# Performance work log

Hardware: AMD Instinct MI355X
Metric: run time of the kernel (lower is better)

## Reference

```python
import jax, jax.numpy as jnp
import numpy as np

B, S, D, H, M = 2, 2048, 1024, 16, 4096  # batch, seqlen, dim, n_heads, max_seq_len
HD = D // H  # head_dim = 64
EPS = 1e-5


def layernorm(x, g, b):
    mu = jnp.mean(x, axis=-1, keepdims=True)
    var = jnp.mean((x - mu) ** 2, axis=-1, keepdims=True)
    return (x - mu) * jax.lax.rsqrt(var + EPS) * g + b


def setup_inputs() -> dict:
    key = jax.random.key(0)
    ks = jax.random.split(key, 5)
    x = jax.random.normal(ks[0], (B, S, D), jnp.float32)
    # causal mask: >=0 -> keep, negative -> drop (forward does att *= mask >= 0)
    i = jnp.arange(S)
    mask = jnp.where(i[None, :] <= i[:, None], 0, -1).astype(jnp.int32)[None, None]
    w1 = jax.random.normal(ks[1], (4 * D, D), jnp.float32) * (D ** -0.5)
    b1 = jnp.zeros((4 * D,), jnp.float32)
    w2 = jax.random.normal(ks[2], (D, D), jnp.float32) * (D ** -0.5)
    b2 = jnp.zeros((D,), jnp.float32)
    g1 = jnp.ones((D,), jnp.float32)
    beta1 = jnp.zeros((D,), jnp.float32)
    g2 = jnp.ones((D,), jnp.float32)
    beta2 = jnp.zeros((D,), jnp.float32)
    pos_w = jax.random.normal(ks[3], (2 * M - 1,), jnp.float32) * 0.02
    return dict(x=x, mask=mask, w1=w1, b1=b1, w2=w2, b2=b2,
                g1=g1, beta1=beta1, g2=g2, beta2=beta2, pos_w=pos_w)


def reference(x, mask, w1, b1, w2, b2, g1, beta1, g2, beta2, pos_w):
    # f1 + silu, split into gate u and q/k/v
    h = jax.nn.silu(x @ w1.T + b1)                      # [B,S,4D]
    u, q, k, v = jnp.split(h, 4, axis=-1)
    to_heads = lambda t: t.reshape(B, S, H, HD).transpose(0, 2, 1, 3)  # [B,H,S,HD]
    u, q, k, v = map(to_heads, (u, q, k, v))
    # relative positional bias: bias[i,j] = pos_w[M-1 + (j - i)]
    rel = jnp.arange(S)[None, :] - jnp.arange(S)[:, None]
    bias = pos_w[M - 1 + rel]                           # [S,S]
    att = jax.nn.silu(jnp.einsum('bhqd,bhkd->bhqk', q, k) + bias)
    att = att * (mask >= 0)                             # [B,H,S,S]
    y = jnp.einsum('bhqk,bhkd->bhqd', att, v) * u
    y = y.transpose(0, 2, 1, 3).reshape(B, S, D)
    y = layernorm(y, g1, beta1)
    y = y @ w2.T + b2
    return layernorm(y + x, g2, beta2)
```

## Files before the change

### kernel.cpp

```cpp
#include <hip/hip_runtime.h>
#include <hip/hip_bf16.h>

#define BN   2
#define SEQ  2048
#define DIM  1024
#define NH   16
#define HD   64
#define D4   4096
#define MAXS 4096

using bf16 = __hip_bfloat16;
typedef __bf16 bf16x8 __attribute__((ext_vector_type(8)));
typedef float  f32x4  __attribute__((ext_vector_type(4)));

__device__ __forceinline__ float bf2f(bf16 v){ return __bfloat162float(v); }
__device__ __forceinline__ bf16  f2bf(float v){ return __float2bfloat16(v); }
__device__ __forceinline__ float silu_f(float v){
  const float e = __expf(-v);
  return v * __builtin_amdgcn_rcpf(1.f + e);
}

__device__ __forceinline__ void async16(void* lds, const void* g){
  __builtin_amdgcn_global_load_lds((const __attribute__((address_space(1))) void*)g,
                                   (__attribute__((address_space(3))) void*)lds, 16, 0, 0);
}
__device__ __forceinline__ f32x4 mfma16(bf16x8 a, bf16x8 b, f32x4 c){
  return __builtin_amdgcn_mfma_f32_16x16x32_bf16(a, b, c, 0, 0, 0);
}

__global__ __launch_bounds__(256) void f2bk3(
    const float* __restrict__ a, bf16* __restrict__ ao, int na,
    const float* __restrict__ b, bf16* __restrict__ bo, int nb,
    const float* __restrict__ c, bf16* __restrict__ co)
{
  int i = (blockIdx.x * 256 + threadIdx.x) * 4;
  const float* in; bf16* out;
  if (i < na){ in = a; out = ao; }
  else if (i < na + nb){ in = b; out = bo; i -= na; }
  else { in = c; out = co; i -= na + nb; }
  const float4 v = *(const float4*)(in + i);
  bf16 t0 = f2bf(v.x), t1 = f2bf(v.y), t2 = f2bf(v.z), t3 = f2bf(v.w);
  ushort4 o;
  o.x = *(unsigned short*)&t0; o.y = *(unsigned short*)&t1;
  o.z = *(unsigned short*)&t2; o.w = *(unsigned short*)&t3;
  *(ushort4*)((unsigned short*)out + i) = o;
}

template<int NTOT>
__global__ __launch_bounds__(256) void gemm_bt(
    const bf16* __restrict__ A, const bf16* __restrict__ W,
    const float* __restrict__ bias, bf16* __restrict__ outb)
{
  constexpr int K = DIM;
  const int ntiles = NTOT / 128;
  const int m0 = (int)(blockIdx.x / ntiles) * 128;
  const int n0 = (int)(blockIdx.x % ntiles) * 128;
  __shared__ bf16 Al[128*32];
  __shared__ bf16 Bl[128*32];
  const int tid = threadIdx.x, wave = tid>>6, lane = tid&63;
  const int quad = lane>>4, l16 = lane&15;
  const int srow = lane>>2;
  const int sg   = ((lane&3) ^ ((lane>>3)&3)) * 8;
  const int wm = (wave>>1)*64, wn = (wave&1)*64;
  const int rkey = ((l16>>1)&3);

  f32x4 acc[4][4];
  #pragma unroll
  for (int i=0;i<4;i++)
    #pragma unroll
    for (int j=0;j<4;j++) acc[i][j] = (f32x4){0.f,0.f,0.f,0.f};

  const bf16* aB = A + m0*K;
  const bf16* wB = W + n0*K;

  for (int k0 = 0; k0 < K; k0 += 32){
    async16(&Al[wave*1024      ], aB + (wave*32      + srow)*K + k0 + sg);
    async16(&Al[wave*1024 + 512], aB + (wave*32 + 16 + srow)*K + k0 + sg);
    async16(&Bl[wave*1024      ], wB + (wave*32      + srow)*K + k0 + sg);
    async16(&Bl[wave*1024 + 512], wB + (wave*32 + 16 + srow)*K + k0 + sg);
    __syncthreads();
    bf16x8 af[4], bv[4];
    #pragma unroll
    for (int mt=0;mt<4;mt++) af[mt] = *(const bf16x8*)&Al[(wm+mt*16+l16)*32 + (quad ^ rkey)*8];
    #pragma unroll
    for (int nt=0;nt<4;nt++) bv[nt] = *(const bf16x8*)&Bl[(wn+nt*16+l16)*32 + (quad ^ rkey)*8];
    #pragma unroll
    for (int mt=0;mt<4;mt++)
      #pragma unroll
      for (int nt=0;nt<4;nt++)
        acc[mt][nt] = mfma16(af[mt], bv[nt], acc[mt][nt]);
    __syncthreads();
  }

  #pragma unroll
  for (int mt=0;mt<4;mt++){
    #pragma unroll
    for (int nt=0;nt<4;nt++){
      const int row = m0 + wm + mt*16 + quad*4;
      const int col = n0 + wn + nt*16 + l16;
      const float bvv = bias[col];
      #pragma unroll
      for (int r=0;r<4;r++){
        float v = silu_f(acc[mt][nt][r] + bvv);
        outb[(row+r)*NTOT + col] = f2bf(v);
      }
    }
  }
}

__global__ __launch_bounds__(256) void gemm_bt2(
    const bf16* __restrict__ A, const bf16* __restrict__ W,
    const float* __restrict__ bias, const float* __restrict__ resid,
    float* __restrict__ outf)
{
  constexpr int K = DIM, NTOT = DIM;
  const int ntiles = NTOT / 64;
  const int m0 = (int)(blockIdx.x / ntiles) * 128;
  const int n0 = (int)(blockIdx.x % ntiles) * 64;
  __shared__ bf16 Al[128*32];
  __shared__ bf16 Bl[64*32];
  const int tid = threadIdx.x, wave = tid>>6, lane = tid&63;
  const int quad = lane>>4, l16 = lane&15;
  const int srow = lane>>2;
  const int sg   = ((lane&3) ^ ((lane>>3)&3)) * 8;
  const int wm = wave*32;
  const int rkey = ((l16>>1)&3);

  f32x4 acc[2][4];
  #pragma unroll
  for (int i=0;i<2;i++)
    #pragma unroll
    for (int j=0;j<4;j++) acc[i][j] = (f32x4){0.f,0.f,0.f,0.f};

  const bf16* aB = A + m0*K;
  const bf16* wB = W + n0*K;

  for (int k0 = 0; k0 < K; k0 += 32){
    async16(&Al[wave*1024      ], aB + (wave*32      + srow)*K + k0 + sg);
    async16(&Al[wave*1024 + 512], aB + (wave*32 + 16 + srow)*K + k0 + sg);
    async16(&Bl[wave*512       ], wB + (wave*16      + srow)*K + k0 + sg);
    __syncthreads();
    bf16x8 af[2], bv[4];
    #pragma unroll
    for (int mt=0;mt<2;mt++) af[mt] = *(const bf16x8*)&Al[(wm+mt*16+l16)*32 + (quad ^ rkey)*8];
    #pragma unroll
    for (int nt=0;nt<4;nt++) bv[nt] = *(const bf16x8*)&Bl[(nt*16+l16)*32 + (quad ^ rkey)*8];
    #pragma unroll
    for (int mt=0;mt<2;mt++)
      #pragma unroll
      for (int nt=0;nt<4;nt++)
        acc[mt][nt] = mfma16(af[mt], bv[nt], acc[mt][nt]);
    __syncthreads();
  }

  #pragma unroll
  for (int mt=0;mt<2;mt++){
    #pragma unroll
    for (int nt=0;nt<4;nt++){
      const int row = m0 + wm + mt*16 + quad*4;
      const int col = n0 + nt*16 + l16;
      const float bvv = bias[col];
      #pragma unroll
      for (int r=0;r<4;r++){
        outf[(row+r)*NTOT + col] = acc[mt][nt][r] + bvv + resid[(row+r)*NTOT + col];
      }
    }
  }
}

__global__ __launch_bounds__(256) void vtrans(const bf16* __restrict__ h, bf16* __restrict__ vt)
{
  __shared__ bf16 t[64][65];
  const int bid = blockIdx.x;
  const int ct = bid & 15;
  const int st = (bid >> 4) & 31;
  const int b  = bid >> 9;
  const int s0 = st*64, c0 = ct*64;
  const int tid = threadIdx.x;
  #pragma unroll
  for (int i=0;i<16;i++){
    int idx = tid + i*256;
    int r = idx >> 6, c = idx & 63;
    t[r][c] = h[(b*SEQ + s0 + r)*D4 + 3*DIM + c0 + c];
  }
  __syncthreads();
  #pragma unroll
  for (int i=0;i<16;i++){
    int idx = tid + i*256;
    int c = idx >> 6, r = idx & 63;
    vt[((b*NH + ct)*HD + c)*SEQ + s0 + r] = t[r][c];
  }
}

__global__ __launch_bounds__(256) void attn(
    const bf16* __restrict__ h, const bf16* __restrict__ vt,
    const float* __restrict__ pw, bf16* __restrict__ y)
{
  const int bid = blockIdx.x;
  const int g  = (bid & 7) + ((bid >> 7) << 3);
  const int qp = (bid >> 3) & 15;
  const int hh = g & 15, b = g >> 4;
  __shared__ bf16 Kl[128*64];
  __shared__ bf16 Vl[64*128];
  __shared__ bf16 Pl[4][16*136];
  __shared__ float pwl[256];
  const int tid = threadIdx.x, wave = tid>>6, lane = tid&63;
  const int quad = lane>>4, l16 = lane&15;

  const bf16* kgb = h + b*SEQ*D4 + 2*DIM + hh*HD;
  const bf16* vgb = vt + (b*NH + hh)*HD*SEQ;
  const int krow8 = lane>>3;
  const int kgo   = ((lane&7) ^ krow8) * 8;
  const int vrow4 = lane>>4;

  #pragma unroll
  for (int pass = 0; pass < 2; ++pass){
    const int qt = pass ? (31 - qp) : qp;
    const int q0 = qt * 64;

    const bf16* qbase = h + (b*SEQ + q0 + wave*16 + l16)*D4 + DIM + hh*HD;
    bf16x8 qf[2];
    qf[0] = *(const bf16x8*)(qbase + quad*8);
    qf[1] = *(const bf16x8*)(qbase + 32 + quad*8);

    f32x4 oacc[4];
    #pragma unroll
    for (int nt=0;nt<4;nt++) oacc[nt] = (f32x4){0.f,0.f,0.f,0.f};

    const int kmax = q0 + 64;
    for (int k0 = 0; k0 < kmax; k0 += 128){
      #pragma unroll
      for (int t=0;t<4;t++)
        async16(&Kl[(wave*32 + t*8)*64], kgb + (k0 + wave*32 + t*8 + krow8)*D4 + kgo);
      #pragma unroll
      for (int t=0;t<4;t++){
        const int vg = ((lane&15) ^ (t*4 + vrow4)) * 8;
        async16(&Vl[(wave*16 + t*4)*128], vgb + (wave*16 + t*4 + vrow4)*SEQ + k0 + vg);
      }
      const int W0 = MAXS - 1 + k0 - q0 - 63;
      if (wave == 0) async16(&pwl[0], pw + W0 + lane*4);
      __syncthreads();

      f32x4 sacc[8];
      #pragma unroll
      for (int nt=0;nt<8;nt++) sacc[nt] = (f32x4){0.f,0.f,0.f,0.f};
      #pragma unroll
      for (int ks=0;ks<2;ks++){
        #pragma unroll
        for (int nt=0;nt<8;nt++){
          bf16x8 kf = *(const bf16x8*)&Kl[(nt*16 + l16)*64 + ((ks*4 + quad) ^ (l16&7))*8];
          sacc[nt] = mfma16(qf[ks], kf, sacc[nt]);
        }
      }
      const int li = wave*16 + quad*4;
      const int dq = q0 - k0;
      #pragma unroll
      for (int nt=0;nt<8;nt++){
        const int lj = nt*16 + l16;
        #pragma unroll
        for (int r=0;r<4;r++){
          const float bias = pwl[lj - (li+r) + 63];
          const float sv = silu_f(sacc[nt][r] + bias);
          const float v = (lj - (li+r) <= dq) ? sv : 0.f;
          Pl[wave][(quad*4+r)*136 + lj] = f2bf(v);
        }
      }

      #pragma unroll
      for (int ks=0;ks<4;ks++){
        bf16x8 pf = *(const bf16x8*)&Pl[wave][l16*136 + ks*32 + quad*8];
        #pragma unroll
        for (int nt=0;nt<4;nt++){
          bf16x8 vf = *(const bf16x8*)&Vl[(nt*16 + l16)*128 + ((ks*4 + quad) ^ l16)*8];
          oacc[nt] = mfma16(pf, vf, oacc[nt]);
        }
      }
      __syncthreads();
    }

    const int qrow = q0 + wave*16 + quad*4;
    #pragma unroll
    for (int nt=0;nt<4;nt++){
      const int c = hh*HD + nt*16 + l16;
      #pragma unroll
      for (int r=0;r<4;r++){
        const int srow = b*SEQ + qrow + r;
        const float uu = bf2f(h[srow*D4 + c]);
        y[srow*DIM + c] = f2bf(oacc[nt][r] * uu);
      }
    }
    __syncthreads();
  }
}

template<bool FP32IN, bool FP32OUT>
__global__ __launch_bounds__(256) void lnorm(const void* __restrict__ in,
    const float* __restrict__ g, const float* __restrict__ be, void* __restrict__ out)
{
  const int row = blockIdx.x;
  const int tid = threadIdx.x, wave = tid>>6, lane = tid&63;
  const int c0 = tid*4;
  float v[4];
  if (FP32IN){
    const float* p = (const float*)in + row*DIM + c0;
    #pragma unroll
    for (int j=0;j<4;j++) v[j] = p[j];
  } else {
    const bf16* p = (const bf16*)in + row*DIM + c0;
    #pragma unroll
    for (int j=0;j<4;j++) v[j] = bf2f(p[j]);
  }
  float s = 0.f, ss = 0.f;
  #pragma unroll
  for (int j=0;j<4;j++){ s += v[j]; ss += v[j]*v[j]; }
  #pragma unroll
  for (int off=32; off>0; off>>=1){
    s  += __shfl_down(s, off);
    ss += __shfl_down(ss, off);
  }
  __shared__ float red[8];
  if (lane==0){ red[wave] = s; red[4+wave] = ss; }
  __syncthreads();
  s  = red[0]+red[1]+red[2]+red[3];
  ss = red[4]+red[5]+red[6]+red[7];
  const float mu   = s * (1.f/DIM);
  const float var  = ss * (1.f/DIM) - mu*mu;
  const float rstd = rsqrtf(var + 1e-5f);
  #pragma unroll
  for (int j=0;j<4;j++){
    const int c = c0 + j;
    const float o = (v[j]-mu)*rstd*g[c] + be[c];
    if (FP32OUT) ((float*)out)[row*DIM + c] = o;
    else         ((bf16*)out)[row*DIM + c] = f2bf(o);
  }
}

extern "C" void kernel_launch(void* const* d_in, const int* in_sizes, int n_in,
                              void* d_out, int out_size, void* d_ws, size_t ws_size,
                              hipStream_t stream)
{
  const float* x   = (const float*)d_in[0];
  const float* w1  = (const float*)d_in[2];
  const float* b1  = (const float*)d_in[3];
  const float* w2  = (const float*)d_in[4];
  const float* b2  = (const float*)d_in[5];
  const float* g1  = (const float*)d_in[6];
  const float* be1 = (const float*)d_in[7];
  const float* g2  = (const float*)d_in[8];
  const float* be2 = (const float*)d_in[9];
  const float* pw  = (const float*)d_in[10];

  char* ws = (char*)d_ws;
  bf16*  h   = (bf16*)(ws);
  bf16*  vt  = (bf16*)(ws + (32u<<20));
  bf16*  y   = (bf16*)(ws + (40u<<20));
  bf16*  xb  = (bf16*)(ws + (48u<<20));
  bf16*  w1b = (bf16*)(ws + (56u<<20));
  bf16*  w2b = (bf16*)(ws + (64u<<20));
  bf16*  l1  = (bf16*)(ws + (32u<<20));
  float* z   = (float*)(ws);

  const int NX  = BN*SEQ*DIM;
  const int NW1 = 4*DIM*DIM;
  const int NW2 = DIM*DIM;
  f2bk3<<<dim3((NX+NW1+NW2)/1024), dim3(256), 0, stream>>>(x, xb, NX, w1, w1b, NW1, w2, w2b);

  gemm_bt<4096><<<dim3(1024), dim3(256), 0, stream>>>(xb, w1b, b1, h);
  vtrans<<<dim3(1024), dim3(256), 0, stream>>>(h, vt);
  attn<<<dim3(512), dim3(256), 0, stream>>>(h, vt, pw, y);
  lnorm<false,false><<<dim3(4096), dim3(256), 0, stream>>>(y, g1, be1, l1);
  gemm_bt2<<<dim3(512), dim3(256), 0, stream>>>(l1, w2b, b2, x, z);
  lnorm<true,true><<<dim3(4096), dim3(256), 0, stream>>>(z, g2, be2, d_out);
}
```

Before: 244.6 us.

## Fuse V transpose into GEMM epilogue and double-buffer attention K/V tiles

The first GEMM now writes the V quarter of its output directly in transposed per-head layout, so the separate vtrans kernel and its extra read and write of V are gone. The attention kernel is restructured: each block processes 128 query rows per pass with 32 rows per wave, over 64-key tiles. K, V and bias tiles are double-buffered in LDS and prefetched with async loads, using explicit waitcnt and barrier instructions. The grid is halved to 256 blocks, which lowers parallelism. Workspace offsets for l1 and z are moved so they no longer alias h and vt.

New measurement: 271.6 us. 1.11x slower.

```diff
diff --git a/kernel.cpp b/kernel.cpp
--- a/kernel.cpp
+++ b/kernel.cpp
@@ -49,7 +49,7 @@
 template<int NTOT>
 __global__ __launch_bounds__(256) void gemm_bt(
     const bf16* __restrict__ A, const bf16* __restrict__ W,
-    const float* __restrict__ bias, bf16* __restrict__ outb)
+    const float* __restrict__ bias, bf16* __restrict__ outb, bf16* __restrict__ vt)
 {
   constexpr int K = DIM;
   const int ntiles = NTOT / 128;
@@ -92,17 +92,42 @@
     __syncthreads();
   }
 
-  #pragma unroll
-  for (int mt=0;mt<4;mt++){
-    #pragma unroll
-    for (int nt=0;nt<4;nt++){
-      const int row = m0 + wm + mt*16 + quad*4;
-      const int col = n0 + wn + nt*16 + l16;
-      const float bvv = bias[col];
-      #pragma unroll
-      for (int r=0;r<4;r++){
-        float v = silu_f(acc[mt][nt][r] + bvv);
-        outb[(row+r)*NTOT + col] = f2bf(v);
+  const bool vtile = (NTOT == 4096) && (n0 >= 3*DIM);
+  if (!vtile){
+    #pragma unroll
+    for (int mt=0;mt<4;mt++){
+      #pragma unroll
+      for (int nt=0;nt<4;nt++){
+        const int row = m0 + wm + mt*16 + quad*4;
+        const int col = n0 + wn + nt*16 + l16;
+        const float bvv = bias[col];
+        #pragma unroll
+        for (int r=0;r<4;r++){
+          float v = silu_f(acc[mt][nt][r] + bvv);
+          outb[(row+r)*NTOT + col] = f2bf(v);
+        }
+      }
+    }
+  } else {
+    #pragma unroll
+    for (int mt=0;mt<4;mt++){
+      #pragma unroll
+      for (int nt=0;nt<4;nt++){
+        const int row = m0 + wm + mt*16 + quad*4;
+        const int colg = n0 + wn + nt*16 + l16;
+        const float bvv = bias[colg];
+        const int col = colg - 3*DIM;
+        const int hh = col >> 6, d = col & 63;
+        const int bb = row >> 11, sl = row & 2047;
+        ushort4 o;
+        float v0 = silu_f(acc[mt][nt][0] + bvv);
+        float v1 = silu_f(acc[mt][nt][1] + bvv);
+        float v2 = silu_f(acc[mt][nt][2] + bvv);
+        float v3 = silu_f(acc[mt][nt][3] + bvv);
+        bf16 t0=f2bf(v0), t1=f2bf(v1), t2=f2bf(v2), t3=f2bf(v3);
+        o.x=*(unsigned short*)&t0; o.y=*(unsigned short*)&t1;
+        o.z=*(unsigned short*)&t2; o.w=*(unsigned short*)&t3;
+        *(ushort4*)&vt[((bb*NH + hh)*HD + d)*SEQ + sl] = o;
       }
     }
   }
@@ -168,125 +193,133 @@
   }
 }
 
-__global__ __launch_bounds__(256) void vtrans(const bf16* __restrict__ h, bf16* __restrict__ vt)
-{
-  __shared__ bf16 t[64][65];
-  const int bid = blockIdx.x;
-  const int ct = bid & 15;
-  const int st = (bid >> 4) & 31;
-  const int b  = bid >> 9;
-  const int s0 = st*64, c0 = ct*64;
-  const int tid = threadIdx.x;
-  #pragma unroll
-  for (int i=0;i<16;i++){
-    int idx = tid + i*256;
-    int r = idx >> 6, c = idx & 63;
-    t[r][c] = h[(b*SEQ + s0 + r)*D4 + 3*DIM + c0 + c];
-  }
-  __syncthreads();
-  #pragma unroll
-  for (int i=0;i<16;i++){
-    int idx = tid + i*256;
-    int c = idx >> 6, r = idx & 63;
-    vt[((b*NH + ct)*HD + c)*SEQ + s0 + r] = t[r][c];
-  }
-}
-
 __global__ __launch_bounds__(256) void attn(
     const bf16* __restrict__ h, const bf16* __restrict__ vt,
     const float* __restrict__ pw, bf16* __restrict__ y)
 {
   const int bid = blockIdx.x;
-  const int g  = (bid & 7) + ((bid >> 7) << 3);
-  const int qp = (bid >> 3) & 15;
+  const int xcd  = bid & 7;
+  const int slot = bid >> 3;
+  const int p    = slot & 7;
+  const int g    = ((slot >> 3) << 3) | xcd;
   const int hh = g & 15, b = g >> 4;
-  __shared__ bf16 Kl[128*64];
-  __shared__ bf16 Vl[64*128];
-  __shared__ bf16 Pl[4][16*136];
-  __shared__ float pwl[256];
+
+  __shared__ bf16 Kl[2][64*64];
+  __shared__ bf16 Vl[2][64*64];
+  __shared__ bf16 Pl[4][32*72];
+  __shared__ float pwl[2][256];
+
   const int tid = threadIdx.x, wave = tid>>6, lane = tid&63;
   const int quad = lane>>4, l16 = lane&15;
+  const int r8 = lane>>3;
+  const int g8 = ((lane&7) ^ r8)*8;
 
   const bf16* kgb = h + b*SEQ*D4 + 2*DIM + hh*HD;
   const bf16* vgb = vt + (b*NH + hh)*HD*SEQ;
-  const int krow8 = lane>>3;
-  const int kgo   = ((lane&7) ^ krow8) * 8;
-  const int vrow4 = lane>>4;
-
-  #pragma unroll
+
   for (int pass = 0; pass < 2; ++pass){
-    const int qt = pass ? (31 - qp) : qp;
-    const int q0 = qt * 64;
-
-    const bf16* qbase = h + (b*SEQ + q0 + wave*16 + l16)*D4 + DIM + hh*HD;
-    bf16x8 qf[2];
-    qf[0] = *(const bf16x8*)(qbase + quad*8);
-    qf[1] = *(const bf16x8*)(qbase + 32 + quad*8);
-
-    f32x4 oacc[4];
-    #pragma unroll
-    for (int nt=0;nt<4;nt++) oacc[nt] = (f32x4){0.f,0.f,0.f,0.f};
-
-    const int kmax = q0 + 64;
-    for (int k0 = 0; k0 < kmax; k0 += 128){
-      #pragma unroll
-      for (int t=0;t<4;t++)
-        async16(&Kl[(wave*32 + t*8)*64], kgb + (k0 + wave*32 + t*8 + krow8)*D4 + kgo);
-      #pragma unroll
-      for (int t=0;t<4;t++){
-        const int vg = ((lane&15) ^ (t*4 + vrow4)) * 8;
-        async16(&Vl[(wave*16 + t*4)*128], vgb + (wave*16 + t*4 + vrow4)*SEQ + k0 + vg);
-      }
-      const int W0 = MAXS - 1 + k0 - q0 - 63;
-      if (wave == 0) async16(&pwl[0], pw + W0 + lane*4);
-      __syncthreads();
-
-      f32x4 sacc[8];
-      #pragma unroll
-      for (int nt=0;nt<8;nt++) sacc[nt] = (f32x4){0.f,0.f,0.f,0.f};
+    const int t = pass ? (15 - p) : p;
+    const int q0 = t * 128;
+
+    bf16x8 qf[2][2];
+    #pragma unroll
+    for (int mt=0;mt<2;mt++){
+      const bf16* qb = h + (b*SEQ + q0 + wave*32 + mt*16 + l16)*D4 + DIM + hh*HD;
+      qf[mt][0] = *(const bf16x8*)(qb + quad*8);
+      qf[mt][1] = *(const bf16x8*)(qb + 32 + quad*8);
+    }
+
+    f32x4 oacc[2][4];
+    #pragma unroll
+    for (int mt=0;mt<2;mt++)
+      #pragma unroll
+      for (int nt=0;nt<4;nt++) oacc[mt][nt] = (f32x4){0.f,0.f,0.f,0.f};
+
+    const int niter = 2*(t+1);
+
+    #pragma unroll
+    for (int tt=0;tt<2;tt++)
+      async16(&Kl[0][(wave*16 + tt*8)*64], kgb + (wave*16 + tt*8 + r8)*D4 + g8);
+    #pragma unroll
+    for (int tt=0;tt<2;tt++)
+      async16(&Vl[0][(wave*16 + tt*8)*64], vgb + (wave*16 + tt*8 + r8)*SEQ + g8);
+    async16(&pwl[0][0], pw + (MAXS-1 - q0 - 127) + lane*4);
+
+    for (int it = 0; it < niter; ++it){
+      const int cur = it & 1;
+      const int k0 = it * 64;
+      if (it + 1 < niter){
+        const int nb = cur ^ 1, kn = k0 + 64;
+        #pragma unroll
+        for (int tt=0;tt<2;tt++)
+          async16(&Kl[nb][(wave*16 + tt*8)*64], kgb + (kn + wave*16 + tt*8 + r8)*D4 + g8);
+        #pragma unroll
+        for (int tt=0;tt<2;tt++)
+          async16(&Vl[nb][(wave*16 + tt*8)*64], vgb + (wave*16 + tt*8 + r8)*SEQ + kn + g8);
+        async16(&pwl[nb][0], pw + (MAXS-1 + kn - q0 - 127) + lane*4);
+        asm volatile("s_waitcnt vmcnt(5)\ns_barrier" ::: "memory");
+      } else {
+        asm volatile("s_waitcnt vmcnt(0)\ns_barrier" ::: "memory");
+      }
+
+      f32x4 sacc[2][4];
+      #pragma unroll
+      for (int mt=0;mt<2;mt++)
+        #pragma unroll
+        for (int nt=0;nt<4;nt++) sacc[mt][nt] = (f32x4){0.f,0.f,0.f,0.f};
       #pragma unroll
       for (int ks=0;ks<2;ks++){
         #pragma unroll
-        for (int nt=0;nt<8;nt++){
-          bf16x8 kf = *(const bf16x8*)&Kl[(nt*16 + l16)*64 + ((ks*4 + quad) ^ (l16&7))*8];
-          sacc[nt] = mfma16(qf[ks], kf, sacc[nt]);
+        for (int nt=0;nt<4;nt++){
+          bf16x8 kf = *(const bf16x8*)&Kl[cur][(nt*16 + l16)*64 + ((ks*4 + quad) ^ (l16&7))*8];
+          sacc[0][nt] = mfma16(qf[0][ks], kf, sacc[0][nt]);
+          sacc[1][nt] = mfma16(qf[1][ks], kf, sacc[1][nt]);
         }
       }
-      const int li = wave*16 + quad*4;
+
       const int dq = q0 - k0;
       #pragma unroll
-      for (int nt=0;nt<8;nt++){
-        const int lj = nt*16 + l16;
+      for (int mt=0;mt<2;mt++){
+        const int i0 = wave*32 + mt*16 + quad*4;
+        #pragma unroll
+        for (int nt=0;nt<4;nt++){
+          const int lj = nt*16 + l16;
+          #pragma unroll
+          for (int r=0;r<4;r++){
+            const int d = lj - (i0 + r);
+            const float bias = pwl[cur][d + 127];
+            const float sv = silu_f(sacc[mt][nt][r] + bias);
+            Pl[wave][(mt*16 + quad*4 + r)*72 + lj] = f2bf((d <= dq) ? sv : 0.f);
+          }
+        }
+      }
+
+      #pragma unroll
+      for (int ks=0;ks<2;ks++){
+        bf16x8 pf0 = *(const bf16x8*)&Pl[wave][(l16     )*72 + ks*32 + quad*8];
+        bf16x8 pf1 = *(const bf16x8*)&Pl[wave][(16 + l16)*72 + ks*32 + quad*8];
+        #pragma unroll
+        for (int nt=0;nt<4;nt++){
+          bf16x8 vf = *(const bf16x8*)&Vl[cur][(nt*16 + l16)*64 + ((ks*4 + quad) ^ (l16&7))*8];
+          oacc[0][nt] = mfma16(pf0, vf, oacc[0][nt]);
+          oacc[1][nt] = mfma16(pf1, vf, oacc[1][nt]);
+        }
+      }
+      asm volatile("s_waitcnt lgkmcnt(0)\ns_barrier" ::: "memory");
+    }
+
+    #pragma unroll
+    for (int mt=0;mt<2;mt++){
+      const int qrow = q0 + wave*32 + mt*16 + quad*4;
+      #pragma unroll
+      for (int nt=0;nt<4;nt++){
+        const int c = hh*HD + nt*16 + l16;
         #pragma unroll
         for (int r=0;r<4;r++){
-          const float bias = pwl[lj - (li+r) + 63];
-          const float sv = silu_f(sacc[nt][r] + bias);
-          const float v = (lj - (li+r) <= dq) ? sv : 0.f;
-          Pl[wave][(quad*4+r)*136 + lj] = f2bf(v);
+          const int srow = b*SEQ + qrow + r;
+          const float uu = bf2f(h[srow*D4 + c]);
+          y[srow*DIM + c] = f2bf(oacc[mt][nt][r] * uu);
         }
-      }
-
-      #pragma unroll
-      for (int ks=0;ks<4;ks++){
-        bf16x8 pf = *(const bf16x8*)&Pl[wave][l16*136 + ks*32 + quad*8];
-        #pragma unroll
-        for (int nt=0;nt<4;nt++){
-          bf16x8 vf = *(const bf16x8*)&Vl[(nt*16 + l16)*128 + ((ks*4 + quad) ^ l16)*8];
-          oacc[nt] = mfma16(pf, vf, oacc[nt]);
-        }
-      }
-      __syncthreads();
-    }
-
-    const int qrow = q0 + wave*16 + quad*4;
-    #pragma unroll
-    for (int nt=0;nt<4;nt++){
-      const int c = hh*HD + nt*16 + l16;
-      #pragma unroll
-      for (int r=0;r<4;r++){
-        const int srow = b*SEQ + qrow + r;
-        const float uu = bf2f(h[srow*D4 + c]);
-        y[srow*DIM + c] = f2bf(oacc[nt][r] * uu);
       }
     }
     __syncthreads();
@@ -357,17 +390,16 @@
   bf16*  xb  = (bf16*)(ws + (48u<<20));
   bf16*  w1b = (bf16*)(ws + (56u<<20));
   bf16*  w2b = (bf16*)(ws + (64u<<20));
-  bf16*  l1  = (bf16*)(ws + (32u<<20));
-  float* z   = (float*)(ws);
+  bf16*  l1  = (bf16*)(ws + (66u<<20));
+  float* z   = (float*)(ws + (74u<<20));
 
   const int NX  = BN*SEQ*DIM;
   const int NW1 = 4*DIM*DIM;
   const int NW2 = DIM*DIM;
   f2bk3<<<dim3((NX+NW1+NW2)/1024), dim3(256), 0, stream>>>(x, xb, NX, w1, w1b, NW1, w2, w2b);
 
-  gemm_bt<4096><<<dim3(1024), dim3(256), 0, stream>>>(xb, w1b, b1, h);
-  vtrans<<<dim3(1024), dim3(256), 0, stream>>>(h, vt);
-  attn<<<dim3(512), dim3(256), 0, stream>>>(h, vt, pw, y);
+  gemm_bt<4096><<<dim3(1024), dim3(256), 0, stream>>>(xb, w1b, b1, h, vt);
+  attn<<<dim3(256), dim3(256), 0, stream>>>(h, vt, pw, y);
   lnorm<false,false><<<dim3(4096), dim3(256), 0, stream>>>(y, g1, be1, l1);
   gemm_bt2<<<dim3(512), dim3(256), 0, stream>>>(l1, w2b, b2, x, z);
   lnorm<true,true><<<dim3(4096), dim3(256), 0, stream>>>(z, g2, be2, d_out);
```

## Fuse V transpose into first GEMM epilogue and store attention probabilities as vectors

Applied to the files above, without the earlier changes.

The first GEMM epilogue now writes the V quarter of its output straight into the transposed per-head layout with 4-wide vector stores, so the separate vtrans kernel and its round trip through global memory are removed. In the attention kernel the QK MFMA operands are swapped so each lane holds four consecutive key positions, which lets the probability tile be written to LDS as one ushort4 per row instead of four scalar stores. Workspace offsets for l1 and z are moved so they no longer alias the vt and h buffers. The V tiles no longer write h, so the GEMM output is partly strided, and the new vt stores stride by SEQ across lanes, which may coalesce poorly.

New measurement: 244.3 us. About the same (-0.1%).

```diff
diff --git a/kernel.cpp b/kernel.cpp
--- a/kernel.cpp
+++ b/kernel.cpp
@@ -49,7 +49,7 @@
 template<int NTOT>
 __global__ __launch_bounds__(256) void gemm_bt(
     const bf16* __restrict__ A, const bf16* __restrict__ W,
-    const float* __restrict__ bias, bf16* __restrict__ outb)
+    const float* __restrict__ bias, bf16* __restrict__ outb, bf16* __restrict__ vt)
 {
   constexpr int K = DIM;
   const int ntiles = NTOT / 128;
@@ -92,17 +92,42 @@
     __syncthreads();
   }
 
-  #pragma unroll
-  for (int mt=0;mt<4;mt++){
-    #pragma unroll
-    for (int nt=0;nt<4;nt++){
-      const int row = m0 + wm + mt*16 + quad*4;
-      const int col = n0 + wn + nt*16 + l16;
-      const float bvv = bias[col];
-      #pragma unroll
-      for (int r=0;r<4;r++){
-        float v = silu_f(acc[mt][nt][r] + bvv);
-        outb[(row+r)*NTOT + col] = f2bf(v);
+  const bool vtile = (NTOT == 4096) && (n0 >= 3*DIM);
+  if (!vtile){
+    #pragma unroll
+    for (int mt=0;mt<4;mt++){
+      #pragma unroll
+      for (int nt=0;nt<4;nt++){
+        const int row = m0 + wm + mt*16 + quad*4;
+        const int col = n0 + wn + nt*16 + l16;
+        const float bvv = bias[col];
+        #pragma unroll
+        for (int r=0;r<4;r++){
+          float v = silu_f(acc[mt][nt][r] + bvv);
+          outb[(row+r)*NTOT + col] = f2bf(v);
+        }
+      }
+    }
+  } else {
+    #pragma unroll
+    for (int mt=0;mt<4;mt++){
+      #pragma unroll
+      for (int nt=0;nt<4;nt++){
+        const int row = m0 + wm + mt*16 + quad*4;
+        const int colg = n0 + wn + nt*16 + l16;
+        const float bvv = bias[colg];
+        const int col = colg - 3*DIM;
+        const int hh = col >> 6, d = col & 63;
+        const int bb = row >> 11, sl = row & 2047;
+        ushort4 o;
+        float v0 = silu_f(acc[mt][nt][0] + bvv);
+        float v1 = silu_f(acc[mt][nt][1] + bvv);
+        float v2 = silu_f(acc[mt][nt][2] + bvv);
+        float v3 = silu_f(acc[mt][nt][3] + bvv);
+        bf16 t0=f2bf(v0), t1=f2bf(v1), t2=f2bf(v2), t3=f2bf(v3);
+        o.x=*(unsigned short*)&t0; o.y=*(unsigned short*)&t1;
+        o.z=*(unsigned short*)&t2; o.w=*(unsigned short*)&t3;
+        *(ushort4*)&vt[((bb*NH + hh)*HD + d)*SEQ + sl] = o;
       }
     }
   }
@@ -168,30 +193,6 @@
   }
 }
 
-__global__ __launch_bounds__(256) void vtrans(const bf16* __restrict__ h, bf16* __restrict__ vt)
-{
-  __shared__ bf16 t[64][65];
-  const int bid = blockIdx.x;
-  const int ct = bid & 15;
-  const int st = (bid >> 4) & 31;
-  const int b  = bid >> 9;
-  const int s0 = st*64, c0 = ct*64;
-  const int tid = threadIdx.x;
-  #pragma unroll
-  for (int i=0;i<16;i++){
-    int idx = tid + i*256;
-    int r = idx >> 6, c = idx & 63;
-    t[r][c] = h[(b*SEQ + s0 + r)*D4 + 3*DIM + c0 + c];
-  }
-  __syncthreads();
-  #pragma unroll
-  for (int i=0;i<16;i++){
-    int idx = tid + i*256;
-    int c = idx >> 6, r = idx & 63;
-    vt[((b*NH + ct)*HD + c)*SEQ + s0 + r] = t[r][c];
-  }
-}
-
 __global__ __launch_bounds__(256) void attn(
     const bf16* __restrict__ h, const bf16* __restrict__ vt,
     const float* __restrict__ pw, bf16* __restrict__ y)
@@ -249,21 +250,29 @@
         #pragma unroll
         for (int nt=0;nt<8;nt++){
           bf16x8 kf = *(const bf16x8*)&Kl[(nt*16 + l16)*64 + ((ks*4 + quad) ^ (l16&7))*8];
-          sacc[nt] = mfma16(qf[ks], kf, sacc[nt]);
+          sacc[nt] = mfma16(kf, qf[ks], sacc[nt]);
         }
       }
-      const int li = wave*16 + quad*4;
+
       const int dq = q0 - k0;
+      const int qrl = wave*16 + l16;
       #pragma unroll
       for (int nt=0;nt<8;nt++){
-        const int lj = nt*16 + l16;
+        const int kb = nt*16 + quad*4;
+        const int d0 = kb - qrl;
+        ushort4 o;
+        bf16 tb[4];
         #pragma unroll
         for (int r=0;r<4;r++){
-          const float bias = pwl[lj - (li+r) + 63];
+          const int d = kb + r - qrl;
+          const float bias = pwl[d + 63];
           const float sv = silu_f(sacc[nt][r] + bias);
-          const float v = (lj - (li+r) <= dq) ? sv : 0.f;
-          Pl[wave][(quad*4+r)*136 + lj] = f2bf(v);
+          tb[r] = f2bf((d <= dq) ? sv : 0.f);
         }
+        (void)d0;
+        o.x=*(unsigned short*)&tb[0]; o.y=*(unsigned short*)&tb[1];
+        o.z=*(unsigned short*)&tb[2]; o.w=*(unsigned short*)&tb[3];
+        *(ushort4*)&Pl[wave][l16*136 + kb] = o;
       }
 
       #pragma unroll
@@ -292,6 +301,7 @@
     __syncthreads();
   }
 }
+
 
 template<bool FP32IN, bool FP32OUT>
 __global__ __launch_bounds__(256) void lnorm(const void* __restrict__ in,
@@ -357,16 +367,15 @@
   bf16*  xb  = (bf16*)(ws + (48u<<20));
   bf16*  w1b = (bf16*)(ws + (56u<<20));
   bf16*  w2b = (bf16*)(ws + (64u<<20));
-  bf16*  l1  = (bf16*)(ws + (32u<<20));
-  float* z   = (float*)(ws);
+  bf16*  l1  = (bf16*)(ws + (66u<<20));
+  float* z   = (float*)(ws + (74u<<20));
 
   const int NX  = BN*SEQ*DIM;
   const int NW1 = 4*DIM*DIM;
   const int NW2 = DIM*DIM;
   f2bk3<<<dim3((NX+NW1+NW2)/1024), dim3(256), 0, stream>>>(x, xb, NX, w1, w1b, NW1, w2, w2b);
 
-  gemm_bt<4096><<<dim3(1024), dim3(256), 0, stream>>>(xb, w1b, b1, h);
-  vtrans<<<dim3(1024), dim3(256), 0, stream>>>(h, vt);
+  gemm_bt<4096><<<dim3(1024), dim3(256), 0, stream>>>(xb, w1b, b1, h, vt);
   attn<<<dim3(512), dim3(256), 0, stream>>>(h, vt, pw, y);
   lnorm<false,false><<<dim3(4096), dim3(256), 0, stream>>>(y, g1, be1, l1);
   gemm_bt2<<<dim3(512), dim3(256), 0, stream>>>(l1, w2b, b2, x, z);
```
